# Kernel optimization log

Hardware: AMD Instinct MI355X
Metric: run time of the kernel (lower is better)

## Reference

```python
import jax, jax.numpy as jnp
import numpy as np

D_MODEL = 512
N_HEADS = 8
HEAD_DIM = D_MODEL // N_HEADS
SCALE = float(np.sqrt(HEAD_DIM))


def setup_inputs() -> dict:
    key = jax.random.key(0)
    k1, k2, k3, k4, k5, k6 = jax.random.split(key, 6)
    B, T, S = 4, 2048, 4096
    query = jax.random.normal(k1, (B, T, D_MODEL), dtype=jnp.float32)
    keys = jax.random.normal(k2, (B, S, D_MODEL), dtype=jnp.float32)
    key_padding_mask = jnp.zeros((B, S), dtype=bool)  # all valid
    # Linear params (torch nn.Linear: y = x @ W.T + b)
    lim = 1.0 / np.sqrt(D_MODEL)
    q_w = jax.random.uniform(k3, (D_MODEL, D_MODEL), jnp.float32, -lim, lim)
    q_b = jax.random.uniform(k4, (D_MODEL,), jnp.float32, -lim, lim)
    k_w = jax.random.uniform(k5, (D_MODEL, D_MODEL), jnp.float32, -lim, lim)
    k_b = jax.random.uniform(k6, (D_MODEL,), jnp.float32, -lim, lim)
    return {"query": query, "keys": keys, "key_padding_mask": key_padding_mask,
            "q_w": q_w, "q_b": q_b, "k_w": k_w, "k_b": k_b}


def reference(query, keys, key_padding_mask, q_w, q_b, k_w, k_b):
    B, T, _ = query.shape
    S = keys.shape[1]
    q = (query @ q_w.T + q_b).reshape(B, T, N_HEADS, HEAD_DIM)
    k = (keys @ k_w.T + k_b).reshape(B, S, N_HEADS, HEAD_DIM)
    # mean over heads of scaled per-head QK^T == single contraction over (h,d)
    # divided by n_heads*scale; avoids materializing [B,H,T,S].
    logits = jnp.einsum('bthd,bshd->bts', q, k) / (N_HEADS * SCALE)
    logits = jnp.where(key_padding_mask[:, None, :], -jnp.inf, logits)
    return logits
```

## Files before the change

kernel.cpp:

```cpp
#include <hip/hip_runtime.h>
#include <hip/hip_bf16.h>

using bf16 = __hip_bfloat16;
typedef __attribute__((ext_vector_type(8))) short short8;
typedef __attribute__((ext_vector_type(16))) float floatx16;

#define NEG_INF (-__builtin_huge_valf())

__device__ __forceinline__ void gld_lds16(const void* g, void* l) {
  __builtin_amdgcn_global_load_lds(
      (const __attribute__((address_space(1))) unsigned int*)g,
      (__attribute__((address_space(3))) unsigned int*)l, 16, 0, 0);
}

__device__ __forceinline__ void cvt8(const float4& a, const float4& b, bf16* t) {
  t[0] = __float2bfloat16(a.x); t[1] = __float2bfloat16(a.y);
  t[2] = __float2bfloat16(a.z); t[3] = __float2bfloat16(a.w);
  t[4] = __float2bfloat16(b.x); t[5] = __float2bfloat16(b.y);
  t[6] = __float2bfloat16(b.z); t[7] = __float2bfloat16(b.w);
}

__global__ void cvt_w(const float* __restrict__ qw, const float* __restrict__ kw,
                      bf16* __restrict__ qwo, bf16* __restrict__ kwo) {
  const int i = blockIdx.x * blockDim.x + threadIdx.x;
  const long e = (long)i << 3;
  const float* src = (e < 262144) ? qw + e : kw + (e - 262144);
  bf16*        dst = (e < 262144) ? qwo + e : kwo + (e - 262144);
  float4 a = *(const float4*)src;
  float4 b = *(const float4*)(src + 4);
  bf16 t[8];
  cvt8(a, b, t);
  *(short8*)dst = *(short8*)t;
}

__device__ __forceinline__ void mfma_tile32(const bf16* sAh, const bf16* sBh,
                                            int wm, int wn, int lane,
                                            floatx16 acc[2][2]) {
  const int fm = lane & 31;
  const int fk = (lane >> 5) * 8;
  #pragma unroll
  for (int ks = 0; ks < 2; ++ks) {
    short8 a0 = *(const short8*)(sAh + (wm +  0 + fm) * 32 + ks * 16 + fk);
    short8 a1 = *(const short8*)(sAh + (wm + 32 + fm) * 32 + ks * 16 + fk);
    short8 b0 = *(const short8*)(sBh + (wn +  0 + fm) * 32 + ks * 16 + fk);
    short8 b1 = *(const short8*)(sBh + (wn + 32 + fm) * 32 + ks * 16 + fk);
    acc[0][0] = __builtin_amdgcn_mfma_f32_32x32x16_bf16(a0, b0, acc[0][0], 0, 0, 0);
    acc[0][1] = __builtin_amdgcn_mfma_f32_32x32x16_bf16(a0, b1, acc[0][1], 0, 0, 0);
    acc[1][0] = __builtin_amdgcn_mfma_f32_32x32x16_bf16(a1, b0, acc[1][0], 0, 0, 0);
    acc[1][1] = __builtin_amdgcn_mfma_f32_32x32x16_bf16(a1, b1, acc[1][1], 0, 0, 0);
  }
}

__global__ __launch_bounds__(256) void proj_fused(const float* __restrict__ X,
                                                  const float* __restrict__ Y,
                                                  const bf16* __restrict__ qw,
                                                  const bf16* __restrict__ kw,
                                                  const float* __restrict__ qb,
                                                  const float* __restrict__ kb,
                                                  bf16* __restrict__ qo,
                                                  bf16* __restrict__ ko) {
  __shared__ bf16 sA[2][128 * 32];
  __shared__ bf16 sB[2][128 * 32];
  const int mt = blockIdx.x;
  const bool isQ = mt < 64;
  const float* A    = isQ ? X  : Y;
  const bf16*  W    = isQ ? qw : kw;
  const float* bias = isQ ? qb : kb;
  bf16* out         = isQ ? qo : ko;
  const int m0 = (isQ ? mt : mt - 64) * 128;
  const int n0 = blockIdx.y * 128;

  const int tid  = threadIdx.x;
  const int lane = tid & 63;
  const int w    = tid >> 6;
  const int wm   = (w >> 1) * 64;
  const int wn   = (w & 1) * 64;
  const int st_row = lane >> 2;
  const int st_col = (lane & 3) * 8;

  floatx16 acc[2][2];
  #pragma unroll
  for (int mi = 0; mi < 2; ++mi)
    #pragma unroll
    for (int ni = 0; ni < 2; ++ni)
      #pragma unroll
      for (int r = 0; r < 16; ++r)
        acc[mi][ni][r] = 0.f;

  for (int kt = 0; kt < 512; kt += 64) {
    #pragma unroll
    for (int h = 0; h < 2; ++h)
      #pragma unroll
      for (int j = 0; j < 2; ++j) {
        const int r = (w << 5) + (j << 4);
        const bf16* gb = W + (size_t)(n0 + r + st_row) * 512 + kt + h * 32 + st_col;
        gld_lds16(gb, &sB[h][r * 32]);
      }
    #pragma unroll
    for (int h = 0; h < 2; ++h)
      #pragma unroll
      for (int j = 0; j < 2; ++j) {
        const int row = (w << 5) + (j << 4) + st_row;
        const float* ga = A + (size_t)(m0 + row) * 512 + kt + h * 32 + st_col;
        float4 a0 = *(const float4*)ga;
        float4 a1 = *(const float4*)(ga + 4);
        bf16 ta[8];
        cvt8(a0, a1, ta);
        *(short8*)(&sA[h][row * 32 + st_col]) = *(short8*)ta;
      }
    __syncthreads();

    #pragma unroll
    for (int h = 0; h < 2; ++h)
      mfma_tile32(sA[h], sB[h], wm, wn, lane, acc);
    __syncthreads();
  }

  const int col = lane & 31;
  const int rhi = (lane >> 5) * 4;
  #pragma unroll
  for (int ni = 0; ni < 2; ++ni) {
    const int gn = n0 + wn + ni * 32 + col;
    const float b = bias[gn];
    #pragma unroll
    for (int mi = 0; mi < 2; ++mi) {
      #pragma unroll
      for (int reg = 0; reg < 16; ++reg) {
        const int row = (reg & 3) + 8 * (reg >> 2) + rhi;
        out[(size_t)(m0 + wm + mi * 32 + row) * 512 + gn] =
            __float2bfloat16(acc[mi][ni][reg] + b);
      }
    }
  }
}

__global__ __launch_bounds__(256) void qk_gemm(const bf16* __restrict__ Q,
                                               const bf16* __restrict__ Kp,
                                               const unsigned char* __restrict__ mask,
                                               float* __restrict__ out) {
  __shared__ bf16 sA[2][128 * 32];
  __shared__ bf16 sB[2][128 * 32];
  const int b = blockIdx.z;
  const bf16* A  = Q  + (size_t)b * 2048 * 512;
  const bf16* Bm = Kp + (size_t)b * 4096 * 512;
  float* ob = out + (size_t)b * 2048 * 4096;
  const unsigned char* mb = mask + (size_t)b * 4096;
  const int m0 = blockIdx.x * 128;
  const int n0 = blockIdx.y * 128;

  const int tid  = threadIdx.x;
  const int lane = tid & 63;
  const int w    = tid >> 6;
  const int wm   = (w >> 1) * 64;
  const int wn   = (w & 1) * 64;
  const int st_row = lane >> 2;
  const int st_col = (lane & 3) * 8;

  floatx16 acc[2][2];
  #pragma unroll
  for (int mi = 0; mi < 2; ++mi)
    #pragma unroll
    for (int ni = 0; ni < 2; ++ni)
      #pragma unroll
      for (int r = 0; r < 16; ++r)
        acc[mi][ni][r] = 0.f;

  for (int kt = 0; kt < 512; kt += 64) {
    #pragma unroll
    for (int h = 0; h < 2; ++h)
      #pragma unroll
      for (int j = 0; j < 2; ++j) {
        const int r = (w << 5) + (j << 4);
        const bf16* ga = A  + (size_t)(m0 + r + st_row) * 512 + kt + h * 32 + st_col;
        const bf16* gb = Bm + (size_t)(n0 + r + st_row) * 512 + kt + h * 32 + st_col;
        gld_lds16(ga, &sA[h][r * 32]);
        gld_lds16(gb, &sB[h][r * 32]);
      }
    __syncthreads();

    #pragma unroll
    for (int h = 0; h < 2; ++h)
      mfma_tile32(sA[h], sB[h], wm, wn, lane, acc);
    __syncthreads();
  }

  const int col = lane & 31;
  const int rhi = (lane >> 5) * 4;
  const float scale = 1.0f / 64.0f;
  #pragma unroll
  for (int ni = 0; ni < 2; ++ni) {
    const int gn = n0 + wn + ni * 32 + col;
    const bool msk = mb[gn] != 0;
    #pragma unroll
    for (int mi = 0; mi < 2; ++mi) {
      #pragma unroll
      for (int reg = 0; reg < 16; ++reg) {
        const int row = (reg & 3) + 8 * (reg >> 2) + rhi;
        ob[(size_t)(m0 + wm + mi * 32 + row) * 4096 + gn] =
            msk ? NEG_INF : acc[mi][ni][reg] * scale;
      }
    }
  }
}

extern "C" void kernel_launch(void* const* d_in, const int* in_sizes, int n_in,
                              void* d_out, int out_size, void* d_ws, size_t ws_size,
                              hipStream_t stream) {
  const float* query = (const float*)d_in[0];
  const float* keys  = (const float*)d_in[1];
  const unsigned char* mask = (const unsigned char*)d_in[2];
  const float* q_w = (const float*)d_in[3];
  const float* q_b = (const float*)d_in[4];
  const float* k_w = (const float*)d_in[5];
  const float* k_b = (const float*)d_in[6];
  float* out = (float*)d_out;

  const int B = 4, T = 2048, S = 4096, D = 512;
  const int nq = B * T * D;
  const int nk = B * S * D;
  const int nw = D * D;

  char* ws = (char*)d_ws;
  bf16* q_proj = (bf16*)(ws);
  bf16* k_proj = (bf16*)(ws + (size_t)nq * 2);
  bf16* qw_bf  = (bf16*)(ws + (size_t)(nq + nk) * 2);
  bf16* kw_bf  = (bf16*)(ws + (size_t)(nq + nk + nw) * 2);

  cvt_w<<<256, 256, 0, stream>>>(q_w, k_w, qw_bf, kw_bf);
  proj_fused<<<dim3(192, D / 128), 256, 0, stream>>>(query, keys, qw_bf, kw_bf,
                                                     q_b, k_b, q_proj, k_proj);
  qk_gemm<<<dim3(T / 128, S / 128, B), 256, 0, stream>>>(q_proj, k_proj, mask, out);
}
```

Baseline: 232.3 us.

## Rewrite QK GEMM with 256x256 tiles, swizzled LDS, double-buffer; pre-convert inputs

Replaces the 128x128 QK GEMM with a 512-thread kernel that computes 256x256 output tiles using 16x16x32 MFMAs. It double-buffers LDS stages with explicit vmcnt waits and barriers, uses XOR-swizzled LDS addressing to avoid bank conflicts, and remaps block IDs for L2 locality. A separate conversion kernel now turns the fp32 activations and weights to bf16 up front, so the projection kernel loads only bf16 through direct-to-LDS loads. The trade-offs are an extra full pass over the inputs plus workspace, and more register pressure in the large-tile kernel.

New measurement: 252.9 us. +8.9%, slower.

```diff
diff --git a/kernel.cpp b/kernel.cpp
--- a/kernel.cpp
+++ b/kernel.cpp
@@ -3,6 +3,7 @@
 
 using bf16 = __hip_bfloat16;
 typedef __attribute__((ext_vector_type(8))) short short8;
+typedef __attribute__((ext_vector_type(4))) float floatx4;
 typedef __attribute__((ext_vector_type(16))) float floatx16;
 
 #define NEG_INF (-__builtin_huge_valf())
@@ -11,6 +12,15 @@
   __builtin_amdgcn_global_load_lds(
       (const __attribute__((address_space(1))) unsigned int*)g,
       (__attribute__((address_space(3))) unsigned int*)l, 16, 0, 0);
+}
+
+template <int N> __device__ __forceinline__ void wait_vm() {
+  asm volatile("s_waitcnt vmcnt(%0)" ::"n"(N) : "memory");
+}
+__device__ __forceinline__ void bar() {
+  asm volatile("" ::: "memory");
+  __builtin_amdgcn_s_barrier();
+  asm volatile("" ::: "memory");
 }
 
 __device__ __forceinline__ void cvt8(const float4& a, const float4& b, bf16* t) {
@@ -20,16 +30,22 @@
   t[6] = __float2bfloat16(b.z); t[7] = __float2bfloat16(b.w);
 }
 
-__global__ void cvt_w(const float* __restrict__ qw, const float* __restrict__ kw,
-                      bf16* __restrict__ qwo, bf16* __restrict__ kwo) {
-  const int i = blockIdx.x * blockDim.x + threadIdx.x;
-  const long e = (long)i << 3;
-  const float* src = (e < 262144) ? qw + e : kw + (e - 262144);
-  bf16*        dst = (e < 262144) ? qwo + e : kwo + (e - 262144);
+__global__ __launch_bounds__(256) void cvt_in(const float* __restrict__ q,
+                                              const float* __restrict__ k,
+                                              const float* __restrict__ qw,
+                                              const float* __restrict__ kw,
+                                              bf16* __restrict__ qo, bf16* __restrict__ ko,
+                                              bf16* __restrict__ qwo, bf16* __restrict__ kwo) {
+  const size_t e = ((size_t)blockIdx.x * 256 + threadIdx.x) * 8;
+  const float* src; bf16* dst;
+  if (e < 4194304)       { src = q  + e;              dst = qo  + e; }
+  else if (e < 12582912) { src = k  + (e - 4194304);  dst = ko  + (e - 4194304); }
+  else if (e < 12845056) { src = qw + (e - 12582912); dst = qwo + (e - 12582912); }
+  else                   { src = kw + (e - 12845056); dst = kwo + (e - 12845056); }
   float4 a = *(const float4*)src;
-  float4 b = *(const float4*)(src + 4);
+  float4 c = *(const float4*)(src + 4);
   bf16 t[8];
-  cvt8(a, b, t);
+  cvt8(a, c, t);
   *(short8*)dst = *(short8*)t;
 }
 
@@ -51,22 +67,22 @@
   }
 }
 
-__global__ __launch_bounds__(256) void proj_fused(const float* __restrict__ X,
-                                                  const float* __restrict__ Y,
-                                                  const bf16* __restrict__ qw,
-                                                  const bf16* __restrict__ kw,
-                                                  const float* __restrict__ qb,
-                                                  const float* __restrict__ kb,
-                                                  bf16* __restrict__ qo,
-                                                  bf16* __restrict__ ko) {
+__global__ __launch_bounds__(256) void proj(const bf16* __restrict__ Xq,
+                                            const bf16* __restrict__ Xk,
+                                            const bf16* __restrict__ qw,
+                                            const bf16* __restrict__ kw,
+                                            const float* __restrict__ qb,
+                                            const float* __restrict__ kb,
+                                            bf16* __restrict__ qo,
+                                            bf16* __restrict__ ko) {
   __shared__ bf16 sA[2][128 * 32];
   __shared__ bf16 sB[2][128 * 32];
   const int mt = blockIdx.x;
   const bool isQ = mt < 64;
-  const float* A    = isQ ? X  : Y;
-  const bf16*  W    = isQ ? qw : kw;
+  const bf16* A    = isQ ? Xq : Xk;
+  const bf16* W    = isQ ? qw : kw;
   const float* bias = isQ ? qb : kb;
-  bf16* out         = isQ ? qo : ko;
+  bf16* outp       = isQ ? qo : ko;
   const int m0 = (isQ ? mt : mt - 64) * 128;
   const int n0 = blockIdx.y * 128;
 
@@ -93,23 +109,12 @@
       #pragma unroll
       for (int j = 0; j < 2; ++j) {
         const int r = (w << 5) + (j << 4);
-        const bf16* gb = W + (size_t)(n0 + r + st_row) * 512 + kt + h * 32 + st_col;
-        gld_lds16(gb, &sB[h][r * 32]);
-      }
-    #pragma unroll
-    for (int h = 0; h < 2; ++h)
-      #pragma unroll
-      for (int j = 0; j < 2; ++j) {
-        const int row = (w << 5) + (j << 4) + st_row;
-        const float* ga = A + (size_t)(m0 + row) * 512 + kt + h * 32 + st_col;
-        float4 a0 = *(const float4*)ga;
-        float4 a1 = *(const float4*)(ga + 4);
-        bf16 ta[8];
-        cvt8(a0, a1, ta);
-        *(short8*)(&sA[h][row * 32 + st_col]) = *(short8*)ta;
+        gld_lds16(A + (size_t)(m0 + r + st_row) * 512 + kt + h * 32 + st_col,
+                  &sA[h][r * 32]);
+        gld_lds16(W + (size_t)(n0 + r + st_row) * 512 + kt + h * 32 + st_col,
+                  &sB[h][r * 32]);
       }
     __syncthreads();
-
     #pragma unroll
     for (int h = 0; h < 2; ++h)
       mfma_tile32(sA[h], sB[h], wm, wn, lane, acc);
@@ -121,85 +126,129 @@
   #pragma unroll
   for (int ni = 0; ni < 2; ++ni) {
     const int gn = n0 + wn + ni * 32 + col;
-    const float b = bias[gn];
-    #pragma unroll
-    for (int mi = 0; mi < 2; ++mi) {
+    const float bv = bias[gn];
+    #pragma unroll
+    for (int mi = 0; mi < 2; ++mi)
       #pragma unroll
       for (int reg = 0; reg < 16; ++reg) {
         const int row = (reg & 3) + 8 * (reg >> 2) + rhi;
-        out[(size_t)(m0 + wm + mi * 32 + row) * 512 + gn] =
-            __float2bfloat16(acc[mi][ni][reg] + b);
-      }
-    }
-  }
-}
-
-__global__ __launch_bounds__(256) void qk_gemm(const bf16* __restrict__ Q,
-                                               const bf16* __restrict__ Kp,
-                                               const unsigned char* __restrict__ mask,
-                                               float* __restrict__ out) {
-  __shared__ bf16 sA[2][128 * 32];
-  __shared__ bf16 sB[2][128 * 32];
-  const int b = blockIdx.z;
-  const bf16* A  = Q  + (size_t)b * 2048 * 512;
-  const bf16* Bm = Kp + (size_t)b * 4096 * 512;
-  float* ob = out + (size_t)b * 2048 * 4096;
-  const unsigned char* mb = mask + (size_t)b * 4096;
-  const int m0 = blockIdx.x * 128;
-  const int n0 = blockIdx.y * 128;
+        outp[(size_t)(m0 + wm + mi * 32 + row) * 512 + gn] =
+            __float2bfloat16(acc[mi][ni][reg] + bv);
+      }
+  }
+}
+
+__global__ __launch_bounds__(512, 2) void qk8(const bf16* __restrict__ Q,
+                                              const bf16* __restrict__ Kp,
+                                              const unsigned char* __restrict__ mask,
+                                              float* __restrict__ out) {
+  __shared__ alignas(16) char smem[2][4][16384];
+
+  const int bid = blockIdx.x;
+  const int sb  = ((bid & 7) << 6) | (bid >> 3);
+  const int b   = sb >> 7;
+  const int mt  = (sb >> 4) & 7;
+  const int nt  = sb & 15;
+
+  const bf16* Qb = Q  + ((size_t)b * 2048 + (size_t)mt * 256) * 512;
+  const bf16* Kb = Kp + ((size_t)b * 4096 + (size_t)nt * 256) * 512;
 
   const int tid  = threadIdx.x;
   const int lane = tid & 63;
   const int w    = tid >> 6;
-  const int wm   = (w >> 1) * 64;
-  const int wn   = (w & 1) * 64;
-  const int st_row = lane >> 2;
-  const int st_col = (lane & 3) * 8;
-
-  floatx16 acc[2][2];
-  #pragma unroll
-  for (int mi = 0; mi < 2; ++mi)
-    #pragma unroll
-    for (int ni = 0; ni < 2; ++ni)
-      #pragma unroll
-      for (int r = 0; r < 16; ++r)
-        acc[mi][ni][r] = 0.f;
-
-  for (int kt = 0; kt < 512; kt += 64) {
-    #pragma unroll
-    for (int h = 0; h < 2; ++h)
-      #pragma unroll
-      for (int j = 0; j < 2; ++j) {
-        const int r = (w << 5) + (j << 4);
-        const bf16* ga = A  + (size_t)(m0 + r + st_row) * 512 + kt + h * 32 + st_col;
-        const bf16* gb = Bm + (size_t)(n0 + r + st_row) * 512 + kt + h * 32 + st_col;
-        gld_lds16(ga, &sA[h][r * 32]);
-        gld_lds16(gb, &sB[h][r * 32]);
-      }
-    __syncthreads();
-
-    #pragma unroll
-    for (int h = 0; h < 2; ++h)
-      mfma_tile32(sA[h], sB[h], wm, wn, lane, acc);
-    __syncthreads();
-  }
-
-  const int col = lane & 31;
-  const int rhi = (lane >> 5) * 4;
-  const float scale = 1.0f / 64.0f;
-  #pragma unroll
-  for (int ni = 0; ni < 2; ++ni) {
-    const int gn = n0 + wn + ni * 32 + col;
-    const bool msk = mb[gn] != 0;
-    #pragma unroll
-    for (int mi = 0; mi < 2; ++mi) {
-      #pragma unroll
-      for (int reg = 0; reg < 16; ++reg) {
-        const int row = (reg & 3) + 8 * (reg >> 2) + rhi;
-        ob[(size_t)(m0 + wm + mi * 32 + row) * 4096 + gn] =
-            msk ? NEG_INF : acc[mi][ni][reg] * scale;
+  const int wm   = w >> 2;
+  const int wn   = w & 3;
+  const int l15  = lane & 15;
+  const int kg   = lane >> 4;
+  const int aoff = l15 * 64 + ((kg << 4) ^ ((l15 & 8) << 2) ^ ((l15 & 2) << 3));
+
+  auto stage = [&](int t) {
+    const int kt = t * 64;
+    char* dst = &smem[t & 1][0][0];
+    #pragma unroll
+    for (int hf = 0; hf < 4; ++hf) {
+      const bf16* src = (hf < 2) ? Qb : Kb;
+      const int rb = (hf & 1) * 128;
+      #pragma unroll
+      for (int L = 0; L < 2; ++L) {
+        const int lin = tid * 16 + L * 8192;
+        const int sub = lin >> 10;
+        const int r   = ((sub >> 1) << 4) | ((lin >> 6) & 15);
+        const int swz = ((r & 8) << 2) ^ ((r & 2) << 3);
+        const int cby = ((sub & 1) << 6) | ((lin & 63) ^ swz);
+        gld_lds16(src + (size_t)(rb + r) * 512 + kt + (cby >> 1),
+                  dst + hf * 16384 + L * 8192 + w * 1024);
       }
     }
+  };
+
+  floatx4 acc[8][4];
+  #pragma unroll
+  for (int i = 0; i < 8; ++i)
+    #pragma unroll
+    for (int j = 0; j < 4; ++j)
+      acc[i][j] = (floatx4){0.f, 0.f, 0.f, 0.f};
+
+  stage(0);
+  stage(1);
+  wait_vm<8>();
+  bar();
+
+  #pragma unroll
+  for (int t = 0; t < 8; ++t) {
+    const char* Ah = &smem[t & 1][wm][0];
+    const char* Bh = &smem[t & 1][2 + (wn >> 1)][0];
+    const int bfb = (wn & 1) * 4;
+    #pragma unroll
+    for (int rh = 0; rh < 2; ++rh) {
+      short8 a[4][2];
+      #pragma unroll
+      for (int fr = 0; fr < 4; ++fr)
+        #pragma unroll
+        for (int ks = 0; ks < 2; ++ks)
+          a[fr][ks] = *(const short8*)(Ah + (rh * 4 + fr) * 2048 + ks * 1024 + aoff);
+      #pragma unroll
+      for (int ch = 0; ch < 2; ++ch) {
+        short8 bb[2][2];
+        #pragma unroll
+        for (int fn = 0; fn < 2; ++fn)
+          #pragma unroll
+          for (int ks = 0; ks < 2; ++ks)
+            bb[fn][ks] = *(const short8*)(Bh + (bfb + ch * 2 + fn) * 2048 + ks * 1024 + aoff);
+        __builtin_amdgcn_s_setprio(1);
+        #pragma unroll
+        for (int fr = 0; fr < 4; ++fr)
+          #pragma unroll
+          for (int fn = 0; fn < 2; ++fn)
+            #pragma unroll
+            for (int ks = 0; ks < 2; ++ks)
+              acc[rh * 4 + fr][ch * 2 + fn] = __builtin_amdgcn_mfma_f32_16x16x32_bf16(
+                  a[fr][ks], bb[fn][ks], acc[rh * 4 + fr][ch * 2 + fn], 0, 0, 0);
+        __builtin_amdgcn_s_setprio(0);
+      }
+    }
+    if (t < 7) {
+      bar();
+      if (t < 6) { stage(t + 2); wait_vm<8>(); }
+      else       { wait_vm<0>(); }
+      bar();
+    }
+  }
+
+  float* ob = out + (size_t)b * 2048 * 4096
+                  + ((size_t)mt * 256 + (size_t)wm * 128) * 4096
+                  + (size_t)nt * 256 + wn * 64;
+  const unsigned char* mb = mask + (size_t)b * 4096 + nt * 256 + wn * 64;
+  #pragma unroll
+  for (int fc = 0; fc < 4; ++fc) {
+    const int c = fc * 16 + l15;
+    const bool msk = mb[c] != 0;
+    #pragma unroll
+    for (int f8 = 0; f8 < 8; ++f8)
+      #pragma unroll
+      for (int r = 0; r < 4; ++r)
+        ob[(size_t)(f8 * 16 + kg * 4 + r) * 4096 + c] =
+            msk ? NEG_INF : acc[f8][fc][r] * (1.f / 64.f);
   }
 }
 
@@ -215,19 +264,20 @@
   const float* k_b = (const float*)d_in[6];
   float* out = (float*)d_out;
 
-  const int B = 4, T = 2048, S = 4096, D = 512;
-  const int nq = B * T * D;
-  const int nk = B * S * D;
-  const int nw = D * D;
+  const size_t nq = 4194304;
+  const size_t nk = 8388608;
+  const size_t nw = 262144;
 
   char* ws = (char*)d_ws;
-  bf16* q_proj = (bf16*)(ws);
-  bf16* k_proj = (bf16*)(ws + (size_t)nq * 2);
-  bf16* qw_bf  = (bf16*)(ws + (size_t)(nq + nk) * 2);
-  bf16* kw_bf  = (bf16*)(ws + (size_t)(nq + nk + nw) * 2);
-
-  cvt_w<<<256, 256, 0, stream>>>(q_w, k_w, qw_bf, kw_bf);
-  proj_fused<<<dim3(192, D / 128), 256, 0, stream>>>(query, keys, qw_bf, kw_bf,
-                                                     q_b, k_b, q_proj, k_proj);
-  qk_gemm<<<dim3(T / 128, S / 128, B), 256, 0, stream>>>(q_proj, k_proj, mask, out);
-}
+  bf16* q_bf   = (bf16*)ws;
+  bf16* k_bf   = (bf16*)(ws + nq * 2);
+  bf16* qw_bf  = (bf16*)(ws + (nq + nk) * 2);
+  bf16* kw_bf  = (bf16*)(ws + (nq + nk + nw) * 2);
+  bf16* q_proj = (bf16*)(ws + (nq + nk + 2 * nw) * 2);
+  bf16* k_proj = (bf16*)(ws + (2 * nq + nk + 2 * nw) * 2);
+
+  cvt_in<<<6400, 256, 0, stream>>>(query, keys, q_w, k_w, q_bf, k_bf, qw_bf, kw_bf);
+  proj<<<dim3(192, 4), 256, 0, stream>>>(q_bf, k_bf, qw_bf, kw_bf, q_b, k_b,
+                                         q_proj, k_proj);
+  qk8<<<512, 512, 0, stream>>>(q_proj, k_proj, mask, out);
+}
```
